# Kernel tuning notes

Measured on AMD Instinct MI355X. Metric: run time of the kernel, lower is better.

The kernel has to match this reference:

```python
import jax, jax.numpy as jnp
import numpy as np

B, C, H, W = 512, 3, 32, 32
N = 50000
D = C * H * W  # 3072


def setup_inputs() -> dict:
    key = jax.random.key(0)
    k1, k2, k3 = jax.random.split(key, 3)
    x = jax.random.normal(k1, (B, C, H, W), dtype=jnp.float32)
    # per-sample noise levels, strictly positive
    sigma = jax.random.uniform(k2, (B,), dtype=jnp.float32, minval=0.5, maxval=2.0)
    # reference dataset, normalized images in [-1, 1], flattened to (N, D)
    y = jax.random.uniform(k3, (N, D), dtype=jnp.float32, minval=-1.0, maxval=1.0)
    return {"x": x, "sigma": sigma, "y": y}


def reference(x, sigma, y):
    Bb, Cc, Hh, Ww = x.shape
    xf = x.astype(jnp.float32).reshape(Bb, Cc * Hh * Ww)          # (B, D)
    s = sigma.astype(jnp.float32).reshape(-1, 1)                  # (B, 1)
    # squared euclidean distance via the GEMM expansion (matches cdist(p=2)**2)
    x2 = jnp.sum(xf * xf, axis=1, keepdims=True)                  # (B, 1)
    y2 = jnp.sum(y * y, axis=1)[None, :]                          # (1, N)
    d2 = jnp.maximum(x2 + y2 - 2.0 * (xf @ y.T), 0.0)             # (B, N)
    logits = -d2 / (2.0 * s * s)                                  # (B, N)
    prob = jax.nn.softmax(logits, axis=1)                         # (B, N)
    denoised = prob @ y                                           # (B, D)
    return denoised.reshape(Bb, Cc, Hh, Ww)
```

## Files before the change

kernel.cpp:

```cpp
#include <hip/hip_runtime.h>


typedef __attribute__((ext_vector_type(4))) float f32x4;
typedef __attribute__((ext_vector_type(4))) int i32x4;
typedef __attribute__((ext_vector_type(4))) char c8x4;
typedef __attribute__((ext_vector_type(4))) unsigned short u16x4;
typedef __attribute__((ext_vector_type(8))) unsigned short u16x8;
typedef __attribute__((ext_vector_type(8))) __bf16 bf16x8;

#define NREAL 50000
#define NP    50176
#define DD    3072
#define BB    512

#define WAIT0  asm volatile("s_waitcnt vmcnt(0)" ::: "memory")
#define VM2    asm volatile("s_waitcnt vmcnt(2)" ::: "memory")
#define VM6    asm volatile("s_waitcnt vmcnt(6)" ::: "memory")
#define VM10   asm volatile("s_waitcnt vmcnt(10)" ::: "memory")
#define LGKM0  asm volatile("s_waitcnt lgkmcnt(0)" ::: "memory")
#define BAR    __builtin_amdgcn_s_barrier()
#define SCHED0 __builtin_amdgcn_sched_barrier(0)

#define SX (6.0f / 127.0f)
#define SY (1.0f / 127.0f)

__device__ __forceinline__ unsigned short f32_bf16_rne(float f) {
  unsigned int u = __float_as_uint(f);
  unsigned int r = 0x7FFFu + ((u >> 16) & 1u);
  return (unsigned short)((u + r) >> 16);
}
__device__ __forceinline__ void gload16(const void* g, void* l) {
  __builtin_amdgcn_global_load_lds(
      (const __attribute__((address_space(1))) void*)g,
      (__attribute__((address_space(3))) void*)l, 16, 0, 0);
}
__device__ __forceinline__ bf16x8 ldsldb(const unsigned short* p) {
  return __builtin_bit_cast(bf16x8, *(const u16x8*)p);
}
__device__ __forceinline__ i32x4 ldsld4(const char* p) {
  return *(const i32x4*)p;
}
__device__ __forceinline__ char q8(float f, float sc) {
  float an = rintf(f * sc);
  an = fminf(127.f, fmaxf(-127.f, an));
  return (char)(int)an;
}

__global__ __launch_bounds__(256) void zero_kernel(f32x4* p) {
  p[(size_t)blockIdx.x * 256 + threadIdx.x] = (f32x4){0.f, 0.f, 0.f, 0.f};
}

__global__ __launch_bounds__(256) void init_rowmin_kernel(int* rowmin) {
  const int i = blockIdx.x * 256 + threadIdx.x;
  if (i < BB) rowmin[i] = 0x7F800000;
}

__global__ __launch_bounds__(256) void prep_x_kernel(
    const float* __restrict__ x, const float* __restrict__ sigma,
    char* __restrict__ ax, char* __restrict__ bx,
    float* __restrict__ x2, float* __restrict__ inv2s2) {
  const int b = blockIdx.x, t = threadIdx.x;
  const f32x4* xr = (const f32x4*)(x + (size_t)b * DD);
  float ssq = 0.f;
#pragma unroll
  for (int i = 0; i < 3; ++i) {
    const int idx = i * 256 + t;
    f32x4 v = xr[idx];
    c8x4 a, bb;
#pragma unroll
    for (int j = 0; j < 4; ++j) {
      float f = v[j];
      ssq += f * f;
      char av = q8(f, 127.0f / 6.0f);
      a[j] = av;
      float r = f - (float)(int)av * SX;
      bb[j] = q8(r, 254.0f * 127.0f / 6.0f);
    }
    *(c8x4*)(ax + (size_t)b * DD + idx * 4) = a;
    *(c8x4*)(bx + (size_t)b * DD + idx * 4) = bb;
  }
  __shared__ float red[4];
#pragma unroll
  for (int off = 32; off > 0; off >>= 1) ssq += __shfl_xor(ssq, off);
  if ((t & 63) == 0) red[t >> 6] = ssq;
  __syncthreads();
  if (t == 0) {
    x2[b] = red[0] + red[1] + red[2] + red[3];
    float s = sigma[b];
    inv2s2[b] = 1.0f / (2.0f * s * s);
  }
}

__global__ __launch_bounds__(256) void prep_y_kernel(
    const float* __restrict__ y, char* __restrict__ ay, char* __restrict__ by,
    unsigned short* __restrict__ yT, float* __restrict__ y2) {
  const int n0 = blockIdx.x * 64;
  const int t = threadIdx.x;
  __shared__ unsigned short T[64][68];
  float ssq[4] = {0.f, 0.f, 0.f, 0.f};
  const int rb = t >> 4;
  const int c4 = (t & 15) * 4;
  const int dr = t >> 2;
  const int nb4 = (t & 3) * 16;

  for (int dp = 0; dp < 48; ++dp) {
    const int d0 = dp * 64;
#pragma unroll
    for (int it = 0; it < 4; ++it) {
      const int r = it * 16 + rb;
      const int n = n0 + r;
      f32x4 v = (n < NREAL) ? *(const f32x4*)(y + (size_t)n * DD + d0 + c4)
                            : (f32x4){0.f, 0.f, 0.f, 0.f};
      c8x4 a, bb;
      u16x4 h;
#pragma unroll
      for (int j = 0; j < 4; ++j) {
        float f = v[j];
        ssq[it] += f * f;
        h[j] = f32_bf16_rne(f);
        char av = q8(f, 127.0f);
        a[j] = av;
        float r2 = f - (float)(int)av * SY;
        bb[j] = q8(r2, 254.0f * 127.0f);
      }
      *(c8x4*)(ay + (size_t)n * DD + d0 + c4) = a;
      *(c8x4*)(by + (size_t)n * DD + d0 + c4) = bb;
      *(u16x4*)(&T[r][c4]) = h;
    }
    __syncthreads();
#pragma unroll
    for (int k = 0; k < 2; ++k) {
      const int nbb = nb4 + k * 8;
      u16x8 o;
#pragma unroll
      for (int j = 0; j < 8; ++j) o[j] = T[nbb + j][dr];
      *(u16x8*)(yT + (size_t)(d0 + dr) * NP + n0 + nbb) = o;
    }
    __syncthreads();
  }
#pragma unroll
  for (int it = 0; it < 4; ++it) {
    float s = ssq[it];
#pragma unroll
    for (int o = 8; o > 0; o >>= 1) s += __shfl_xor(s, o, 16);
    if ((t & 15) == 0) y2[n0 + it * 16 + rb] = s;
  }
}

__global__ __launch_bounds__(512, 2) void qk_kernel(
    const char* __restrict__ ay, const char* __restrict__ by,
    const char* __restrict__ ax, const char* __restrict__ bx,
    const float* __restrict__ x2, const float* __restrict__ inv2s2,
    const float* __restrict__ y2, float* __restrict__ S, int* __restrict__ rowmin) {
  const int orig = blockIdx.x;
  const int virt = (orig & 7) * 98 + (orig >> 3);
  const int mt = virt & 1, nt = virt >> 1;
  const int m0 = mt * 256, n0 = nt * 128;
  const int t = threadIdx.x, lane = t & 63, w = t >> 6;
  const int wm = w >> 1, wn = w & 1;
  const int l15 = lane & 15;
  const int cs = ((lane >> 4) ^ ((l15 >> 1) & 3)) * 16;

  __shared__ __align__(16) char L[3][49152];

  i32x4 acc1[4][4] = {};
  i32x4 acc2[4][4] = {};

  const int srow = t >> 2;
  const int sc = ((t & 3) ^ ((t >> 3) & 3)) * 16;
  const int sdst = t * 16;

  const char* pax0 = ax + (size_t)(m0 + srow) * DD + sc;
  const char* pax1 = ax + (size_t)(m0 + srow + 128) * DD + sc;
  const char* pbx0 = bx + (size_t)(m0 + srow) * DD + sc;
  const char* pbx1 = bx + (size_t)(m0 + srow + 128) * DD + sc;
  const char* pay = ay + (size_t)(n0 + srow) * DD + sc;
  const char* pby = by + (size_t)(n0 + srow) * DD + sc;

  auto SA = [&](int buf) {
    char* base = L[buf];
    gload16(pax0, base + sdst);
    gload16(pax1, base + 8192 + sdst);
    gload16(pbx0, base + 16384 + sdst);
    gload16(pbx1, base + 16384 + 8192 + sdst);
    pax0 += 64; pax1 += 64; pbx0 += 64; pbx1 += 64;
  };
  auto SB = [&](int buf) {
    char* base = L[buf];
    gload16(pay, base + 32768 + sdst);
    gload16(pby, base + 40960 + sdst);
    pay += 64; pby += 64;
  };

  i32x4 ayf[4], byf[4], axf[2], bxf[2];
  auto RB = [&](int buf) {
    const char* base = L[buf];
#pragma unroll
    for (int nf = 0; nf < 4; ++nf) {
      const int row = wn * 64 + nf * 16 + l15;
      ayf[nf] = ldsld4(base + 32768 + row * 64 + cs);
      byf[nf] = ldsld4(base + 40960 + row * 64 + cs);
    }
  };
  auto RA = [&](int buf, int mh) {
    const char* base = L[buf];
#pragma unroll
    for (int m2 = 0; m2 < 2; ++m2) {
      const int row = wm * 64 + (mh * 2 + m2) * 16 + l15;
      axf[m2] = ldsld4(base + row * 64 + cs);
      bxf[m2] = ldsld4(base + 16384 + row * 64 + cs);
    }
  };
  auto MF = [&](int mh) {
    __builtin_amdgcn_s_setprio(1);
#pragma unroll
    for (int m2 = 0; m2 < 2; ++m2) {
      const int mf = mh * 2 + m2;
#pragma unroll
      for (int nf = 0; nf < 4; ++nf) {
        acc1[mf][nf] = __builtin_amdgcn_mfma_i32_16x16x64_i8(axf[m2], ayf[nf], acc1[mf][nf], 0, 0, 0);
        acc2[mf][nf] = __builtin_amdgcn_mfma_i32_16x16x64_i8(axf[m2], byf[nf], acc2[mf][nf], 0, 0, 0);
        acc2[mf][nf] = __builtin_amdgcn_mfma_i32_16x16x64_i8(bxf[m2], ayf[nf], acc2[mf][nf], 0, 0, 0);
      }
    }
    __builtin_amdgcn_s_setprio(0);
  };

  SA(0); SB(0); SA(1); SB(1);

  for (int k = 0; k < 48; ++k) {
    const int buf = k % 3;
    BAR;
    if (k <= 45) SA((k + 2) % 3);
    if (k <= 45) { VM10; } else if (k == 46) { VM6; } else { WAIT0; }
    BAR;
    RB(buf); RA(buf, 0);
    MF(0);
    if (k <= 45) SB((k + 2) % 3);
    RA(buf, 1);
    MF(1);
  }

  const float C1 = 6.0f / 16129.0f;
  const float C2 = C1 / 254.0f;
  float rmv[4][4];
#pragma unroll
  for (int mf = 0; mf < 4; ++mf)
#pragma unroll
    for (int i = 0; i < 4; ++i) rmv[mf][i] = 3.0e38f;

#pragma unroll
  for (int nf = 0; nf < 4; ++nf) {
    const int col = n0 + wn * 64 + nf * 16 + l15;
    const bool ok = (col < NREAL);
    const float yy = ok ? y2[col] : 0.f;
#pragma unroll
    for (int mf = 0; mf < 4; ++mf) {
#pragma unroll
      for (int i = 0; i < 4; ++i) {
        const int row = m0 + wm * 64 + mf * 16 + ((lane >> 4) * 4) + i;
        float v = 3.0e38f;
        if (ok) {
          float dot = C1 * (float)acc1[mf][nf][i] + C2 * (float)acc2[mf][nf][i];
          float d2 = fmaxf(x2[row] + yy - 2.0f * dot, 0.0f);
          v = d2 * inv2s2[row];
          rmv[mf][i] = fminf(rmv[mf][i], v);
        }
        S[(size_t)row * NP + col] = v;
      }
    }
  }
#pragma unroll
  for (int mf = 0; mf < 4; ++mf)
#pragma unroll
    for (int i = 0; i < 4; ++i) {
      float v = rmv[mf][i];
#pragma unroll
      for (int o = 1; o < 16; o <<= 1) v = fminf(v, __shfl_xor(v, o));
      rmv[mf][i] = v;
    }
  if (l15 == 0) {
#pragma unroll
    for (int mf = 0; mf < 4; ++mf)
#pragma unroll
      for (int i = 0; i < 4; ++i) {
        const int row = m0 + wm * 64 + mf * 16 + ((lane >> 4) * 4) + i;
        atomicMin(rowmin + row, __float_as_int(rmv[mf][i]));
      }
  }
}

__global__ __launch_bounds__(256) void softmax_kernel(
    const float* __restrict__ S, const int* __restrict__ rowmin,
    unsigned short* __restrict__ P, float* __restrict__ invs) {
  const int b = blockIdx.x, t = threadIdx.x;
  const f32x4* row = (const f32x4*)(S + (size_t)b * NP);
  const float rm = __int_as_float(rowmin[b]);
  __shared__ float red[4];

  unsigned short* pr = P + (size_t)b * NP;
  float sum = 0.f;
#pragma unroll 4
  for (int i = 0; i < 49; ++i) {
    const int e = i * 256 + t;
    f32x4 v = row[e];
    float e0 = __expf(rm - v[0]), e1 = __expf(rm - v[1]);
    float e2 = __expf(rm - v[2]), e3 = __expf(rm - v[3]);
    sum += e0 + e1 + e2 + e3;
    u16x4 o;
    o[0] = f32_bf16_rne(e0); o[1] = f32_bf16_rne(e1);
    o[2] = f32_bf16_rne(e2); o[3] = f32_bf16_rne(e3);
    *(u16x4*)(pr + (size_t)e * 4) = o;
  }
#pragma unroll
  for (int off = 32; off > 0; off >>= 1) sum += __shfl_xor(sum, off);
  if ((t & 63) == 0) red[t >> 6] = sum;
  __syncthreads();
  if (t == 0) invs[b] = 1.0f / (red[0] + red[1] + red[2] + red[3]);
}

__global__ __launch_bounds__(512, 2) void pv_kernel(
    const unsigned short* __restrict__ yT, const unsigned short* __restrict__ P,
    const float* __restrict__ invs, float* __restrict__ out) {
  const int orig = blockIdx.x;
  const int virt = (orig & 7) * 96 + (orig >> 3);
  const int sp = virt / 24;
  const int r24 = virt % 24;
  const int dt = r24 >> 1, mt = r24 & 1;
  const int m0 = mt * 256, d0 = dt * 256;
  const int k0t = sp * 24 + (sp < 16 ? sp : 16);
  const int NT = 24 + (sp < 16 ? 1 : 0);

  const int t = threadIdx.x;
  const int lane = t & 63, w = t >> 6;
  const int wm = w >> 2, wn = w & 3;
  const int l15 = lane & 15;
  const int h3 = (l15 >> 1) & 7;
  const int cs0 = ((lane >> 4) ^ h3) * 8;
  const int cs1 = ((4 + (lane >> 4)) ^ h3) * 8;

  __shared__ __align__(16) unsigned short L[2][2][16384];

  f32x4 acc[8][4] = {};

  const int srow8 = t >> 3;
  const int sc = ((t & 7) ^ ((t >> 4) & 7)) * 8;
  const int sdst = t * 8;

  const size_t kbeg = (size_t)k0t * 64;
  const unsigned short* pA[4];
  pA[0] = P + (size_t)(m0 + srow8) * NP + kbeg + sc;
  pA[1] = P + (size_t)(m0 + srow8 + 128) * NP + kbeg + sc;
  pA[2] = P + (size_t)(m0 + srow8 + 64) * NP + kbeg + sc;
  pA[3] = P + (size_t)(m0 + srow8 + 192) * NP + kbeg + sc;
  const unsigned short* pB[4];
#pragma unroll
  for (int r = 0; r < 4; ++r)
    pB[r] = yT + (size_t)(d0 + srow8 + r * 64) * NP + kbeg + sc;

  auto SB01 = [&](int b) {
    gload16(pB[0], &L[b][1][sdst]); gload16(pB[1], &L[b][1][sdst + 4096]);
    pB[0] += 64; pB[1] += 64;
  };
  auto SB23 = [&](int b) {
    gload16(pB[2], &L[b][1][sdst + 8192]); gload16(pB[3], &L[b][1][sdst + 12288]);
    pB[2] += 64; pB[3] += 64;
  };
  auto SA01 = [&](int b) {
    gload16(pA[0], &L[b][0][sdst]); gload16(pA[1], &L[b][0][sdst + 4096]);
    pA[0] += 64; pA[1] += 64;
  };
  auto SA23 = [&](int b) {
    gload16(pA[2], &L[b][0][sdst + 8192]); gload16(pA[3], &L[b][0][sdst + 12288]);
    pA[2] += 64; pA[3] += 64;
  };

  bf16x8 a[4], bv[4];
  auto RA = [&](int b, int mh, int cs) {
#pragma unroll
    for (int m4 = 0; m4 < 4; ++m4)
      a[m4] = ldsldb(&L[b][0][(mh * 128 + wm * 64 + m4 * 16 + l15) * 64 + cs]);
  };
  auto RB = [&](int b, int cs) {
#pragma unroll
    for (int nf = 0; nf < 4; ++nf)
      bv[nf] = ldsldb(&L[b][1][(wn * 64 + nf * 16 + l15) * 64 + cs]);
  };
  auto MF = [&](int mh) {
    __builtin_amdgcn_s_setprio(1);
#pragma unroll
    for (int m4 = 0; m4 < 4; ++m4)
#pragma unroll
      for (int nf = 0; nf < 4; ++nf)
        acc[mh * 4 + m4][nf] = __builtin_amdgcn_mfma_f32_16x16x32_bf16(
            a[m4], bv[nf], acc[mh * 4 + m4][nf], 0, 0, 0);
    __builtin_amdgcn_s_setprio(0);
  };

  SB01(0); SB23(0); SA01(0); SA23(0);
  WAIT0; BAR;

  for (int k = 0; k < NT - 1; ++k) {
    const int b = k & 1, nb = b ^ 1;
    RB(b, cs0); RA(b, 0, cs0);
    SB01(nb);
    BAR; LGKM0; SCHED0;
    MF(0);
    VM2;
    BAR;
    RA(b, 1, cs0);
    SB23(nb);
    BAR; LGKM0; SCHED0;
    MF(1);
    BAR;
    RB(b, cs1); RA(b, 0, cs1);
    SA01(nb);
    BAR; LGKM0; SCHED0;
    MF(0);
    BAR;
    RA(b, 1, cs1);
    SA23(nb);
    BAR; LGKM0; SCHED0;
    MF(1);
    VM2;
    BAR;
  }
  {
    const int b = (NT - 1) & 1;
    RB(b, cs0); RA(b, 0, cs0);
    BAR; LGKM0; SCHED0;
    MF(0);
    WAIT0;
    BAR;
    RA(b, 1, cs0);
    LGKM0; SCHED0;
    MF(1);
    RB(b, cs1); RA(b, 0, cs1);
    LGKM0; SCHED0;
    MF(0);
    RA(b, 1, cs1);
    LGKM0; SCHED0;
    MF(1);
  }

#pragma unroll
  for (int mi = 0; mi < 8; ++mi)
#pragma unroll
    for (int i = 0; i < 4; ++i) {
      const int row = m0 + wm * 128 + mi * 16 + ((lane >> 4) * 4) + i;
      const float scale = invs[row];
#pragma unroll
      for (int nf = 0; nf < 4; ++nf) {
        const int col = d0 + wn * 64 + nf * 16 + l15;
        unsafeAtomicAdd(out + (size_t)row * DD + col, acc[mi][nf][i] * scale);
      }
    }
}

extern "C" void kernel_launch(void* const* d_in, const int* in_sizes, int n_in,
                              void* d_out, int out_size, void* d_ws, size_t ws_size,
                              hipStream_t stream) {
  const float* x = (const float*)d_in[0];
  const float* sigma = (const float*)d_in[1];
  const float* y = (const float*)d_in[2];
  float* out = (float*)d_out;
  char* ws = (char*)d_ws;

  size_t off = 0;
  float* S = (float*)(ws + off);                      off += (size_t)BB * NP * 4;
  char* ay = (char*)(ws + off);                       off += (size_t)NP * DD;
  char* by = (char*)(ws + off);                       off += (size_t)NP * DD;
  unsigned short* P = (unsigned short*)by;
  char* ax = (char*)(ws + off);                       off += (size_t)BB * DD;
  char* bx = (char*)(ws + off);                       off += (size_t)BB * DD;
  float* y2 = (float*)(ws + off);                     off += (size_t)NP * 4;
  float* x2 = (float*)(ws + off);                     off += 512 * 4;
  float* inv2s2 = (float*)(ws + off);                 off += 512 * 4;
  float* invs = (float*)(ws + off);                   off += 512 * 4;
  int* rowmin = (int*)(ws + off);                     off += 512 * 4;
  unsigned short* yT = (unsigned short*)(ws + off);   off += (size_t)DD * NP * 2;
  off += 65536;
  if (ws_size < off) return;

  zero_kernel<<<dim3(1536), dim3(256), 0, stream>>>((f32x4*)out);
  init_rowmin_kernel<<<dim3(2), dim3(256), 0, stream>>>(rowmin);
  prep_x_kernel<<<dim3(512), dim3(256), 0, stream>>>(x, sigma, ax, bx, x2, inv2s2);
  prep_y_kernel<<<dim3(NP / 64), dim3(256), 0, stream>>>(y, ay, by, yT, y2);
  qk_kernel<<<dim3(784), dim3(512), 0, stream>>>(ay, by, ax, bx, x2, inv2s2, y2, S, rowmin);
  softmax_kernel<<<dim3(512), dim3(256), 0, stream>>>(S, rowmin, P, invs);
  pv_kernel<<<dim3(768), dim3(512), 0, stream>>>(yT, P, invs, out);
}
```

Baseline: 998.9 us.

## Split y preprocessing into per-row quantize kernel and tiled transpose kernel

The old prep_y kernel ran 784 blocks, each looping serially over all 48 column tiles, which gave little parallelism for a large streaming pass. It is replaced by a per-row quantize kernel (one block per row, writing int8 pairs, a row-major bf16 copy and the squared norm) and a separate transpose kernel with 784×48 independent tiles. This adds an extra write and read of the bf16 copy of y, about 300 MB, in exchange for much higher occupancy and better-coalesced reads. The bf16 buffer reuses the score-matrix workspace region, since S is written only after the transpose finishes.

Measured after the change: 989.9 us. About the same (-0.9%).

```diff
diff --git a/kernel.cpp b/kernel.cpp
--- a/kernel.cpp
+++ b/kernel.cpp
@@ -91,59 +91,73 @@
   }
 }
 
-__global__ __launch_bounds__(256) void prep_y_kernel(
+__global__ __launch_bounds__(256) void quant_y_kernel(
     const float* __restrict__ y, char* __restrict__ ay, char* __restrict__ by,
-    unsigned short* __restrict__ yT, float* __restrict__ y2) {
-  const int n0 = blockIdx.x * 64;
+    unsigned short* __restrict__ ybf, float* __restrict__ y2) {
+  const int n = blockIdx.x, t = threadIdx.x;
+  if (n >= NREAL) {
+    c8x4 z = {0, 0, 0, 0};
+    u16x4 zh = {0, 0, 0, 0};
+#pragma unroll
+    for (int i = 0; i < 3; ++i) {
+      const int idx = i * 256 + t;
+      *(c8x4*)(ay + (size_t)n * DD + idx * 4) = z;
+      *(c8x4*)(by + (size_t)n * DD + idx * 4) = z;
+      *(u16x4*)(ybf + (size_t)n * DD + idx * 4) = zh;
+    }
+    if (t == 0) y2[n] = 0.f;
+    return;
+  }
+  const f32x4* yr = (const f32x4*)(y + (size_t)n * DD);
+  float ssq = 0.f;
+#pragma unroll
+  for (int i = 0; i < 3; ++i) {
+    const int idx = i * 256 + t;
+    f32x4 v = yr[idx];
+    c8x4 a, bb;
+    u16x4 h;
+#pragma unroll
+    for (int j = 0; j < 4; ++j) {
+      float f = v[j];
+      ssq += f * f;
+      h[j] = f32_bf16_rne(f);
+      char av = q8(f, 127.0f);
+      a[j] = av;
+      float r2 = f - (float)(int)av * SY;
+      bb[j] = q8(r2, 254.0f * 127.0f);
+    }
+    *(c8x4*)(ay + (size_t)n * DD + idx * 4) = a;
+    *(c8x4*)(by + (size_t)n * DD + idx * 4) = bb;
+    *(u16x4*)(ybf + (size_t)n * DD + idx * 4) = h;
+  }
+  __shared__ float red[4];
+#pragma unroll
+  for (int off = 32; off > 0; off >>= 1) ssq += __shfl_xor(ssq, off);
+  if ((t & 63) == 0) red[t >> 6] = ssq;
+  __syncthreads();
+  if (t == 0) y2[n] = red[0] + red[1] + red[2] + red[3];
+}
+
+__global__ __launch_bounds__(256) void tr_y_kernel(
+    const unsigned short* __restrict__ ybf, unsigned short* __restrict__ yT) {
+  const int bn = blockIdx.x % 784, bd = blockIdx.x / 784;
+  const int n0 = bn * 64, d0 = bd * 64;
+  __shared__ unsigned short T[64][72];
   const int t = threadIdx.x;
-  __shared__ unsigned short T[64][68];
-  float ssq[4] = {0.f, 0.f, 0.f, 0.f};
-  const int rb = t >> 4;
-  const int c4 = (t & 15) * 4;
+  const int r = t >> 2, cc = (t & 3) * 16;
+  u16x8 v0 = *(const u16x8*)(ybf + (size_t)(n0 + r) * DD + d0 + cc);
+  u16x8 v1 = *(const u16x8*)(ybf + (size_t)(n0 + r) * DD + d0 + cc + 8);
+  *(u16x8*)(&T[r][cc]) = v0;
+  *(u16x8*)(&T[r][cc + 8]) = v1;
+  __syncthreads();
   const int dr = t >> 2;
-  const int nb4 = (t & 3) * 16;
-
-  for (int dp = 0; dp < 48; ++dp) {
-    const int d0 = dp * 64;
-#pragma unroll
-    for (int it = 0; it < 4; ++it) {
-      const int r = it * 16 + rb;
-      const int n = n0 + r;
-      f32x4 v = (n < NREAL) ? *(const f32x4*)(y + (size_t)n * DD + d0 + c4)
-                            : (f32x4){0.f, 0.f, 0.f, 0.f};
-      c8x4 a, bb;
-      u16x4 h;
-#pragma unroll
-      for (int j = 0; j < 4; ++j) {
-        float f = v[j];
-        ssq[it] += f * f;
-        h[j] = f32_bf16_rne(f);
-        char av = q8(f, 127.0f);
-        a[j] = av;
-        float r2 = f - (float)(int)av * SY;
-        bb[j] = q8(r2, 254.0f * 127.0f);
-      }
-      *(c8x4*)(ay + (size_t)n * DD + d0 + c4) = a;
-      *(c8x4*)(by + (size_t)n * DD + d0 + c4) = bb;
-      *(u16x4*)(&T[r][c4]) = h;
-    }
-    __syncthreads();
-#pragma unroll
-    for (int k = 0; k < 2; ++k) {
-      const int nbb = nb4 + k * 8;
-      u16x8 o;
-#pragma unroll
-      for (int j = 0; j < 8; ++j) o[j] = T[nbb + j][dr];
-      *(u16x8*)(yT + (size_t)(d0 + dr) * NP + n0 + nbb) = o;
-    }
-    __syncthreads();
-  }
-#pragma unroll
-  for (int it = 0; it < 4; ++it) {
-    float s = ssq[it];
-#pragma unroll
-    for (int o = 8; o > 0; o >>= 1) s += __shfl_xor(s, o, 16);
-    if ((t & 15) == 0) y2[n0 + it * 16 + rb] = s;
+#pragma unroll
+  for (int k = 0; k < 2; ++k) {
+    const int nb = ((t & 3) * 2 + k) * 8;
+    u16x8 o;
+#pragma unroll
+    for (int j = 0; j < 8; ++j) o[j] = T[nb + j][dr];
+    *(u16x8*)(yT + (size_t)(d0 + dr) * NP + n0 + nb) = o;
   }
 }
 
@@ -467,7 +481,9 @@
   char* ws = (char*)d_ws;
 
   size_t off = 0;
-  float* S = (float*)(ws + off);                      off += (size_t)BB * NP * 4;
+  unsigned short* ybf = (unsigned short*)(ws);
+  float* S = (float*)(ws);
+  off += (size_t)NP * DD * 2;
   char* ay = (char*)(ws + off);                       off += (size_t)NP * DD;
   char* by = (char*)(ws + off);                       off += (size_t)NP * DD;
   unsigned short* P = (unsigned short*)by;
@@ -485,7 +501,8 @@
   zero_kernel<<<dim3(1536), dim3(256), 0, stream>>>((f32x4*)out);
   init_rowmin_kernel<<<dim3(2), dim3(256), 0, stream>>>(rowmin);
   prep_x_kernel<<<dim3(512), dim3(256), 0, stream>>>(x, sigma, ax, bx, x2, inv2s2);
-  prep_y_kernel<<<dim3(NP / 64), dim3(256), 0, stream>>>(y, ay, by, yT, y2);
+  quant_y_kernel<<<dim3(NP), dim3(256), 0, stream>>>(y, ay, by, ybf, y2);
+  tr_y_kernel<<<dim3(784 * 48), dim3(256), 0, stream>>>(ybf, yT);
   qk_kernel<<<dim3(784), dim3(512), 0, stream>>>(ay, by, ax, bx, x2, inv2s2, y2, S, rowmin);
   softmax_kernel<<<dim3(512), dim3(256), 0, stream>>>(S, rowmin, P, invs);
   pv_kernel<<<dim3(768), dim3(512), 0, stream>>>(yT, P, invs, out);
```
